# Performance work log

Measured on AMD Instinct MI355X. Metric: run time of the kernel, lower is better.

## Reference

```python
import jax, jax.numpy as jnp
import numpy as np

CODEBOOK_SIZE = 65536
HIDDEN = 768
B, L = 2, 2048
COMMITMENT_COST = 0.25


def setup_inputs() -> dict:
    key = jax.random.key(0)
    k1, k2 = jax.random.split(key)
    embeddings = jax.random.normal(k1, (B, L, HIDDEN), dtype=jnp.float32)
    # torch init: uniform(-1/K, 1/K)
    bound = 1.0 / CODEBOOK_SIZE
    codebook = jax.random.uniform(k2, (CODEBOOK_SIZE, HIDDEN), dtype=jnp.float32,
                                  minval=-bound, maxval=bound)
    return {"embeddings": embeddings, "codebook": codebook}


def reference(embeddings, codebook):
    Bv, Lv, D = embeddings.shape
    z = embeddings.reshape(-1, D)  # (N, D)
    # pairwise squared distances: z^2 + e^2 - 2 z e^T  -> (N, K)
    z_sq = jnp.sum(z * z, axis=-1, keepdims=True)          # (N, 1)
    e_sq = jnp.sum(codebook * codebook, axis=-1)[None, :]  # (1, K)
    distances = z_sq + e_sq - 2.0 * (z @ codebook.T)       # (N, K)
    codes = jnp.argmin(distances, axis=-1)                 # (N,)
    quantized = codebook[codes]                            # (N, D) gather
    # VQ loss: codebook loss + commitment loss (stop-grads as in torch .detach())
    codebook_loss = jnp.mean((quantized - jax.lax.stop_gradient(z)) ** 2)
    commitment_loss = jnp.mean((z - jax.lax.stop_gradient(quantized)) ** 2)
    vq_loss = codebook_loss + COMMITMENT_COST * commitment_loss
    # straight-through estimator
    quantized_ste = z + jax.lax.stop_gradient(quantized - z)
    return (codes.reshape(Bv, Lv),
            quantized_ste.reshape(Bv, Lv, D),
            vq_loss)
```

## Files before the change

kernel.cpp:

```cpp
#include <hip/hip_runtime.h>
#include <cfloat>
#include <cstdint>

#define NROWS  4096
#define DIM    768
#define KCODES 65536

#define TM 128
#define TC 128
#define BK1 128
#define SA 40
#define CAP 1024
#define DELTA 3.0e-4f

#define WS_ZSQ    0
#define WS_RUNMIN 16384
#define WS_CNT    32768
#define WS_CODESI 49152
#define WS_LOSS   65536
#define WS_LIST   131072
#define WS_AH     (WS_LIST + (size_t)NROWS*CAP*4)
#define WS_BH     (WS_AH + (size_t)NROWS*DIM*2)
#define WS_NEED   (WS_BH + (size_t)KCODES*DIM*2)

typedef _Float16 half_t;
typedef _Float16 half8 __attribute__((ext_vector_type(8)));
typedef float    f32x4 __attribute__((ext_vector_type(4)));

__device__ __forceinline__ void gld16(half_t* lds, const half_t* g) {
  __builtin_amdgcn_global_load_lds(
      (const __attribute__((address_space(1))) unsigned int*)g,
      (__attribute__((address_space(3))) unsigned int*)lds, 16, 0, 0);
}

__global__ void k0_zsq(const float* __restrict__ z, float* __restrict__ zsq,
                       unsigned int* __restrict__ runmin, int* __restrict__ cnt,
                       unsigned long long* __restrict__ keys, double* __restrict__ loss) {
  const int wave = threadIdx.x >> 6, lane = threadIdx.x & 63;
  const int row = blockIdx.x * 4 + wave;
  const float* zr = z + (size_t)row * DIM;
  float s = 0.f;
  #pragma unroll
  for (int i = 0; i < DIM / 64; ++i) { float v = zr[lane + i * 64]; s = fmaf(v, v, s); }
  #pragma unroll
  for (int off = 32; off; off >>= 1) s += __shfl_xor(s, off, 64);
  if (lane == 0) zsq[row] = s;
  const int gid = blockIdx.x * 256 + threadIdx.x;
  if (gid < NROWS) {
    runmin[gid] = 0x7f7fffffu;
    cnt[gid] = 0;
    keys[gid] = ~0ull;
  }
  if (gid == 0) *loss = 0.0;
}

__global__ void k_conv(const float* __restrict__ src, half_t* __restrict__ h,
                       int n8, float prescale) {
  const int i = blockIdx.x * 256 + threadIdx.x;
  if (i >= n8) return;
  float4 v0 = ((const float4*)src)[2 * i];
  float4 v1 = ((const float4*)src)[2 * i + 1];
  float a[8] = {v0.x, v0.y, v0.z, v0.w, v1.x, v1.y, v1.z, v1.w};
  half8 hi;
  #pragma unroll
  for (int j = 0; j < 8; ++j) hi[j] = (half_t)(a[j] * prescale);
  ((half8*)h)[i] = hi;
}

__global__ __launch_bounds__(256, 2) void k1_s1(
    const half_t* __restrict__ Ahg, const half_t* __restrict__ Bhg,
    const float* __restrict__ zsq, unsigned int* __restrict__ runmin,
    int* __restrict__ cnt, int* __restrict__ list) {
  __shared__ __align__(16) half_t sA[TM * BK1];
  __shared__ __align__(16) half_t sB[TC * BK1];
  __shared__ float lzs[TM];
  __shared__ float redD[TM][2];
  __shared__ float lbound[TM];

  const int tid = threadIdx.x;
  const int row0  = blockIdx.x * TM;
  const int code0 = blockIdx.y * TC;
  const int wave = tid >> 6, lane = tid & 63;
  const int wm = wave & 1, wn = wave >> 1;
  const int q = lane >> 4, l16 = lane & 15;

  if (tid < TM) lzs[tid] = zsq[row0 + tid];

  f32x4 acc[16];
  #pragma unroll
  for (int i = 0; i < 16; ++i) acc[i] = (f32x4){0.f, 0.f, 0.f, 0.f};

  for (int kd = 0; kd < DIM; kd += BK1) {
    __syncthreads();
    #pragma unroll
    for (int i = 0; i < 8; ++i) {
      const int sid  = i * 256 + tid;
      const int lrow = sid >> 4;
      const int kp   = sid & 15;
      const int klog = kp ^ (lrow & 7);
      const int loff = lrow * BK1 + kp * 8;
      gld16(&sA[loff], Ahg + (size_t)(row0 + lrow) * DIM + kd + klog * 8);
      gld16(&sB[loff], Bhg + (size_t)(code0 + lrow) * DIM + kd + klog * 8);
    }
    __syncthreads();

    #pragma unroll
    for (int s = 0; s < 4; ++s) {
      const int klq = s * 4 + q;
      half8 fa[4], fb[4];
      #pragma unroll
      for (int t = 0; t < 4; ++t) {
        const int ar = wm * 64 + t * 16 + l16;
        fa[t] = *(const half8*)&sA[ar * BK1 + (klq ^ (ar & 7)) * 8];
        const int br = wn * 64 + t * 16 + l16;
        fb[t] = *(const half8*)&sB[br * BK1 + (klq ^ (br & 7)) * 8];
      }
      #pragma unroll
      for (int tm = 0; tm < 4; ++tm)
        #pragma unroll
        for (int tn = 0; tn < 4; ++tn)
          acc[tm * 4 + tn] = __builtin_amdgcn_mfma_f32_16x16x32_f16(fa[tm], fb[tn], acc[tm * 4 + tn], 0, 0, 0);
    }
  }

  const float c2 = -4.8828125e-4f;
  #pragma unroll
  for (int tm = 0; tm < 4; ++tm)
    #pragma unroll
    for (int reg = 0; reg < 4; ++reg) {
      const float zs = lzs[wm * 64 + tm * 16 + q * 4 + reg];
      #pragma unroll
      for (int tn = 0; tn < 4; ++tn)
        acc[tm * 4 + tn][reg] = fmaf(c2, acc[tm * 4 + tn][reg], zs);
    }

  #pragma unroll
  for (int tm = 0; tm < 4; ++tm)
    #pragma unroll
    for (int reg = 0; reg < 4; ++reg) {
      float m = acc[tm * 4 + 0][reg];
      #pragma unroll
      for (int tn = 1; tn < 4; ++tn) m = fminf(m, acc[tm * 4 + tn][reg]);
      #pragma unroll
      for (int off = 8; off; off >>= 1) m = fminf(m, __shfl_xor(m, off, 64));
      if (l16 == 0) redD[wm * 64 + tm * 16 + q * 4 + reg][wn] = m;
    }
  __syncthreads();
  if (tid < TM) {
    const float lm = fminf(redD[tid][0], redD[tid][1]);
    const unsigned rg = runmin[row0 + tid];
    atomicMin(&runmin[row0 + tid], __float_as_uint(lm));
    lbound[tid] = fminf(lm, __uint_as_float(rg)) + DELTA;
  }
  __syncthreads();

  #pragma unroll
  for (int tm = 0; tm < 4; ++tm)
    #pragma unroll
    for (int reg = 0; reg < 4; ++reg) {
      const int row_b = wm * 64 + tm * 16 + q * 4 + reg;
      const float b = lbound[row_b];
      #pragma unroll
      for (int tn = 0; tn < 4; ++tn) {
        const float d = acc[tm * 4 + tn][reg];
        if (d <= b) {
          const int grow = row0 + row_b;
          const int pos = atomicAdd(&cnt[grow], 1);
          if (pos < CAP) list[(size_t)grow * CAP + pos] = code0 + wn * 64 + tn * 16 + l16;
        }
      }
    }
}

__global__ void k_refine(const float* __restrict__ z, const float* __restrict__ cb,
                         const float* __restrict__ zsq, const int* __restrict__ cnt,
                         const int* __restrict__ list, float* __restrict__ out_codes,
                         int* __restrict__ codes_i) {
  const int r = blockIdx.x;
  const int wave = threadIdx.x >> 6, lane = threadIdx.x & 63;
  __shared__ unsigned long long wbest[4];
  int n = cnt[r]; if (n > CAP) n = CAP;
  const bool empty = (n == 0); if (empty) n = 1;
  unsigned long long best = ~0ull;
  const float* zr = z + (size_t)r * DIM;
  for (int ci = wave; ci < n; ci += 4) {
    const int idx = empty ? 0 : list[(size_t)r * CAP + ci];
    const float* cr = cb + (size_t)idx * DIM;
    double s = 0.0;
    #pragma unroll
    for (int j = 0; j < 12; ++j) {
      const int k = lane + j * 64;
      s += (double)zr[k] * (double)cr[k];
    }
    #pragma unroll
    for (int off = 32; off; off >>= 1) s += __shfl_xor(s, off, 64);
    const float d = (float)((double)zsq[r] - 2.0 * s);
    const unsigned long long key =
        ((unsigned long long)__float_as_uint(d) << 32) | (unsigned)idx;
    if (key < best) best = key;
  }
  if (lane == 0) wbest[wave] = best;
  __syncthreads();
  if (threadIdx.x == 0) {
    unsigned long long b = wbest[0];
    #pragma unroll
    for (int w = 1; w < 4; ++w) if (wbest[w] < b) b = wbest[w];
    const int idx = (int)(unsigned)(b & 0xffffffffull);
    codes_i[r] = idx;
    out_codes[r] = (float)idx;
  }
}

__global__ __launch_bounds__(256, 2) void k1_mfma(
    const float* __restrict__ z, const float* __restrict__ cb,
    const float* __restrict__ zsq, unsigned long long* __restrict__ keys) {
  __shared__ half_t Ah[TM * SA], Al[TM * SA], Bh[TC * SA], Bl[TC * SA];
  __shared__ float lzs[TM];
  __shared__ float redD[TM][2];
  __shared__ int   redI[TM][2];

  const int tid  = threadIdx.x;
  const int row0  = blockIdx.x * TM;
  const int code0 = blockIdx.y * TC;
  const int wave = tid >> 6, lane = tid & 63;
  const int wm = wave & 1, wn = wave >> 1;
  const int q = lane >> 4, l16 = lane & 15;

  if (tid < TM) lzs[tid] = zsq[row0 + tid];

  const int srow = tid >> 2;
  const int sko  = (tid & 3) * 8;

  f32x4 acc0[16], acc1[16];
  #pragma unroll
  for (int i = 0; i < 16; ++i) {
    acc0[i] = (f32x4){0.f, 0.f, 0.f, 0.f};
    acc1[i] = (f32x4){0.f, 0.f, 0.f, 0.f};
  }

  const float* zp = z  + (size_t)row0  * DIM;
  const float* bp = cb + (size_t)code0 * DIM;

  for (int kd = 0; kd < DIM; kd += 32) {
    __syncthreads();
    #pragma unroll
    for (int s = 0; s < 2; ++s) {
      const int r = srow + s * 64;
      const float* srca = zp + (size_t)r * DIM + kd + sko;
      float4 v0 = *(const float4*)srca;
      float4 v1 = *(const float4*)(srca + 4);
      float a[8] = {v0.x, v0.y, v0.z, v0.w, v1.x, v1.y, v1.z, v1.w};
      half8 hi, lo;
      #pragma unroll
      for (int j = 0; j < 8; ++j) {
        half_t h = (half_t)a[j];
        hi[j] = h;
        lo[j] = (half_t)((a[j] - (float)h) * 4096.f);
      }
      *(half8*)&Ah[r * SA + sko] = hi;
      *(half8*)&Al[r * SA + sko] = lo;
      const float* srcb = bp + (size_t)r * DIM + kd + sko;
      v0 = *(const float4*)srcb; v1 = *(const float4*)(srcb + 4);
      float b[8] = {v0.x, v0.y, v0.z, v0.w, v1.x, v1.y, v1.z, v1.w};
      #pragma unroll
      for (int j = 0; j < 8; ++j) {
        float bs = b[j] * 4096.f;
        half_t h = (half_t)bs;
        hi[j] = h;
        lo[j] = (half_t)((bs - (float)h) * 4096.f);
      }
      *(half8*)&Bh[r * SA + sko] = hi;
      *(half8*)&Bl[r * SA + sko] = lo;
    }
    __syncthreads();

    half8 fa_h[4], fa_l[4], fb_h[4], fb_l[4];
    #pragma unroll
    for (int t = 0; t < 4; ++t) {
      const int ar = (wm * 64 + t * 16 + l16) * SA + q * 8;
      fa_h[t] = *(const half8*)&Ah[ar];
      fa_l[t] = *(const half8*)&Al[ar];
      const int br = (wn * 64 + t * 16 + l16) * SA + q * 8;
      fb_h[t] = *(const half8*)&Bh[br];
      fb_l[t] = *(const half8*)&Bl[br];
    }
    #pragma unroll
    for (int tm = 0; tm < 4; ++tm)
      #pragma unroll
      for (int tn = 0; tn < 4; ++tn) {
        const int i = tm * 4 + tn;
        acc0[i] = __builtin_amdgcn_mfma_f32_16x16x32_f16(fa_h[tm], fb_h[tn], acc0[i], 0, 0, 0);
        acc1[i] = __builtin_amdgcn_mfma_f32_16x16x32_f16(fa_l[tm], fb_h[tn], acc1[i], 0, 0, 0);
        acc1[i] = __builtin_amdgcn_mfma_f32_16x16x32_f16(fa_h[tm], fb_l[tn], acc1[i], 0, 0, 0);
      }
  }

  const float c1 = 2.44140625e-4f;
  const float c2 = -4.8828125e-4f;
  #pragma unroll
  for (int tm = 0; tm < 4; ++tm) {
    #pragma unroll
    for (int reg = 0; reg < 4; ++reg) {
      const int row_b = wm * 64 + tm * 16 + q * 4 + reg;
      const float zs = lzs[row_b];
      float bd = FLT_MAX; int bi = 0x7fffffff;
      #pragma unroll
      for (int tn = 0; tn < 4; ++tn) {
        const int i = tm * 4 + tn;
        float v = fmaf(c1, acc1[i][reg], acc0[i][reg]);
        float d = fmaf(c2, v, zs);
        const int ci = code0 + wn * 64 + tn * 16 + l16;
        if (d < bd || (d == bd && ci < bi)) { bd = d; bi = ci; }
      }
      #pragma unroll
      for (int off = 8; off; off >>= 1) {
        float od = __shfl_xor(bd, off, 64);
        int   oi = __shfl_xor(bi, off, 64);
        if (od < bd || (od == bd && oi < bi)) { bd = od; bi = oi; }
      }
      if (l16 == 0) { redD[row_b][wn] = bd; redI[row_b][wn] = bi; }
    }
  }
  __syncthreads();
  if (tid < TM) {
    float d0 = redD[tid][0]; int i0 = redI[tid][0];
    float d1 = redD[tid][1]; int i1 = redI[tid][1];
    if (d1 < d0 || (d1 == d0 && i1 < i0)) { d0 = d1; i0 = i1; }
    unsigned long long key = ((unsigned long long)__float_as_uint(d0) << 32) | (unsigned int)i0;
    atomicMin(&keys[row0 + tid], key);
  }
}

__global__ void k2_codes(const unsigned long long* __restrict__ keys,
                         float* __restrict__ out_codes, int* __restrict__ codes_i) {
  const int r = blockIdx.x * 256 + threadIdx.x;
  const int idx = (int)(unsigned int)(keys[r] & 0xffffffffull);
  out_codes[r] = (float)idx;
  codes_i[r] = idx;
}

__global__ void k3_quant_loss(const float* __restrict__ z, const float* __restrict__ cb,
                              const int* __restrict__ codes, float* __restrict__ outq,
                              double* __restrict__ loss) {
  const int gid = blockIdx.x * blockDim.x + threadIdx.x;
  const int e0 = gid * 4;
  const int row = e0 / DIM;
  const int col = e0 - row * DIM;
  const int c = codes[row];
  const float4 zv = *(const float4*)(z + e0);
  const float4 qv = *(const float4*)(cb + (size_t)c * DIM + col);
  float d0 = qv.x - zv.x, d1 = qv.y - zv.y, d2 = qv.z - zv.z, d3 = qv.w - zv.w;
  float4 ov = { zv.x + d0, zv.y + d1, zv.z + d2, zv.w + d3 };
  *(float4*)(outq + e0) = ov;
  double s = (double)(d0 * d0) + (double)(d1 * d1) + (double)(d2 * d2) + (double)(d3 * d3);
  #pragma unroll
  for (int off = 32; off; off >>= 1) s += __shfl_xor(s, off, 64);
  __shared__ double wsum[4];
  const int wave = threadIdx.x >> 6, lane = threadIdx.x & 63;
  if (lane == 0) wsum[wave] = s;
  __syncthreads();
  if (threadIdx.x == 0) atomicAdd(loss, wsum[0] + wsum[1] + wsum[2] + wsum[3]);
}

__global__ void k4_final(const double* __restrict__ loss, float* __restrict__ out) {
  float m = (float)(*loss / ((double)NROWS * (double)DIM));
  out[0] = m + 0.25f * m;
}

extern "C" void kernel_launch(void* const* d_in, const int* in_sizes, int n_in,
                              void* d_out, int out_size, void* d_ws, size_t ws_size,
                              hipStream_t stream) {
  const float* z  = (const float*)d_in[0];
  const float* cb = (const float*)d_in[1];
  float* out = (float*)d_out;
  char* ws = (char*)d_ws;
  float*  zsq = (float*)(ws + WS_ZSQ);
  unsigned int* runmin = (unsigned int*)(ws + WS_RUNMIN);
  int* cnt     = (int*)(ws + WS_CNT);
  int* codes_i = (int*)(ws + WS_CODESI);
  double* loss = (double*)(ws + WS_LOSS);
  int* list    = (int*)(ws + WS_LIST);
  unsigned long long* keys = (unsigned long long*)(ws + WS_LIST);

  k0_zsq<<<NROWS / 4, 256, 0, stream>>>(z, zsq, runmin, cnt, keys, loss);

  dim3 g1(NROWS / TM, KCODES / TC);
  if (ws_size >= WS_NEED) {
    half_t* Ahg = (half_t*)(ws + WS_AH);
    half_t* Bhg = (half_t*)(ws + WS_BH);
    k_conv<<<(NROWS * DIM / 8 + 255) / 256, 256, 0, stream>>>(z, Ahg, NROWS * DIM / 8, 1.0f);
    k_conv<<<(KCODES * DIM / 8 + 255) / 256, 256, 0, stream>>>(cb, Bhg, KCODES * DIM / 8, 4096.0f);
    k1_s1<<<g1, 256, 0, stream>>>(Ahg, Bhg, zsq, runmin, cnt, list);
    k_refine<<<NROWS, 256, 0, stream>>>(z, cb, zsq, cnt, list, out, codes_i);
  } else {
    k1_mfma<<<g1, 256, 0, stream>>>(z, cb, zsq, keys);
    k2_codes<<<NROWS / 256, 256, 0, stream>>>(keys, out, codes_i);
  }

  k3_quant_loss<<<(NROWS * DIM / 4) / 256, 256, 0, stream>>>(z, cb, codes_i, out + NROWS, loss);

  k4_final<<<1, 1, 0, stream>>>(loss, out + NROWS + (size_t)NROWS * DIM);
}
```

Baseline: 1.115 ms.

## Fuse zsq with z conversion, shrink GEMM K-tile, fuse quantize/loss into refine

The z-squared-norm pass now also converts z to fp16, which removes a separate conversion launch. The refine kernel now writes the straight-through quantized output and accumulates the loss itself, which removes the separate quantize/loss kernel. The screening GEMM uses a 64-wide K tile with a new swizzled load mapping and launch bounds raised to 4 blocks per CU, halving LDS per block so more blocks can be resident. The candidate list cap doubles, and refine stages the z row in LDS and uses float4 loads. Risks are register spilling at the higher occupancy target and more loop iterations and syncs per K step.

```diff
diff --git a/kernel.cpp b/kernel.cpp
--- a/kernel.cpp
+++ b/kernel.cpp
@@ -8,9 +8,9 @@
 
 #define TM 128
 #define TC 128
-#define BK1 128
+#define BK 64
 #define SA 40
-#define CAP 1024
+#define CAP 2048
 #define DELTA 3.0e-4f
 
 #define WS_ZSQ    0
@@ -24,6 +24,7 @@
 #define WS_NEED   (WS_BH + (size_t)KCODES*DIM*2)
 
 typedef _Float16 half_t;
+typedef _Float16 half4 __attribute__((ext_vector_type(4)));
 typedef _Float16 half8 __attribute__((ext_vector_type(8)));
 typedef float    f32x4 __attribute__((ext_vector_type(4)));
 
@@ -33,29 +34,31 @@
       (__attribute__((address_space(3))) unsigned int*)lds, 16, 0, 0);
 }
 
-__global__ void k0_zsq(const float* __restrict__ z, float* __restrict__ zsq,
-                       unsigned int* __restrict__ runmin, int* __restrict__ cnt,
-                       unsigned long long* __restrict__ keys, double* __restrict__ loss) {
+__global__ void k_convA(const float* __restrict__ z, half_t* __restrict__ h,
+                        float* __restrict__ zsq, unsigned int* __restrict__ runmin,
+                        int* __restrict__ cnt, double* __restrict__ loss) {
   const int wave = threadIdx.x >> 6, lane = threadIdx.x & 63;
   const int row = blockIdx.x * 4 + wave;
-  const float* zr = z + (size_t)row * DIM;
+  const float4* zr = (const float4*)(z + (size_t)row * DIM);
+  half_t* hr = h + (size_t)row * DIM;
   float s = 0.f;
   #pragma unroll
-  for (int i = 0; i < DIM / 64; ++i) { float v = zr[lane + i * 64]; s = fmaf(v, v, s); }
+  for (int p = 0; p < 3; ++p) {
+    float4 v = zr[lane + p * 64];
+    s = fmaf(v.x, v.x, s); s = fmaf(v.y, v.y, s);
+    s = fmaf(v.z, v.z, s); s = fmaf(v.w, v.w, s);
+    half4 hv = { (half_t)v.x, (half_t)v.y, (half_t)v.z, (half_t)v.w };
+    *(half4*)(hr + (lane + p * 64) * 4) = hv;
+  }
   #pragma unroll
   for (int off = 32; off; off >>= 1) s += __shfl_xor(s, off, 64);
   if (lane == 0) zsq[row] = s;
   const int gid = blockIdx.x * 256 + threadIdx.x;
-  if (gid < NROWS) {
-    runmin[gid] = 0x7f7fffffu;
-    cnt[gid] = 0;
-    keys[gid] = ~0ull;
-  }
+  if (gid < NROWS) { runmin[gid] = 0x7f7fffffu; cnt[gid] = 0; }
   if (gid == 0) *loss = 0.0;
 }
 
-__global__ void k_conv(const float* __restrict__ src, half_t* __restrict__ h,
-                       int n8, float prescale) {
+__global__ void k_convB(const float* __restrict__ src, half_t* __restrict__ h, int n8) {
   const int i = blockIdx.x * 256 + threadIdx.x;
   if (i >= n8) return;
   float4 v0 = ((const float4*)src)[2 * i];
@@ -63,16 +66,16 @@
   float a[8] = {v0.x, v0.y, v0.z, v0.w, v1.x, v1.y, v1.z, v1.w};
   half8 hi;
   #pragma unroll
-  for (int j = 0; j < 8; ++j) hi[j] = (half_t)(a[j] * prescale);
+  for (int j = 0; j < 8; ++j) hi[j] = (half_t)(a[j] * 4096.f);
   ((half8*)h)[i] = hi;
 }
 
-__global__ __launch_bounds__(256, 2) void k1_s1(
+__global__ __launch_bounds__(256, 4) void k1_s1(
     const half_t* __restrict__ Ahg, const half_t* __restrict__ Bhg,
     const float* __restrict__ zsq, unsigned int* __restrict__ runmin,
     int* __restrict__ cnt, int* __restrict__ list) {
-  __shared__ __align__(16) half_t sA[TM * BK1];
-  __shared__ __align__(16) half_t sB[TC * BK1];
+  __shared__ __align__(16) half_t sA[TM * BK];
+  __shared__ __align__(16) half_t sB[TC * BK];
   __shared__ float lzs[TM];
   __shared__ float redD[TM][2];
   __shared__ float lbound[TM];
@@ -86,34 +89,35 @@
 
   if (tid < TM) lzs[tid] = zsq[row0 + tid];
 
+  const int sr = lane >> 3;
+  const int ss = lane & 7;
+  const int gswz = ss ^ sr;
+
   f32x4 acc[16];
   #pragma unroll
   for (int i = 0; i < 16; ++i) acc[i] = (f32x4){0.f, 0.f, 0.f, 0.f};
 
-  for (int kd = 0; kd < DIM; kd += BK1) {
+  for (int kd = 0; kd < DIM; kd += BK) {
     __syncthreads();
     #pragma unroll
-    for (int i = 0; i < 8; ++i) {
-      const int sid  = i * 256 + tid;
-      const int lrow = sid >> 4;
-      const int kp   = sid & 15;
-      const int klog = kp ^ (lrow & 7);
-      const int loff = lrow * BK1 + kp * 8;
-      gld16(&sA[loff], Ahg + (size_t)(row0 + lrow) * DIM + kd + klog * 8);
-      gld16(&sB[loff], Bhg + (size_t)(code0 + lrow) * DIM + kd + klog * 8);
+    for (int i = 0; i < 4; ++i) {
+      const int r = wave * 32 + i * 8 + sr;
+      const int loff = r * BK + ss * 8;
+      gld16(&sA[loff], Ahg + (size_t)(row0  + r) * DIM + kd + gswz * 8);
+      gld16(&sB[loff], Bhg + (size_t)(code0 + r) * DIM + kd + gswz * 8);
     }
     __syncthreads();
 
     #pragma unroll
-    for (int s = 0; s < 4; ++s) {
+    for (int s = 0; s < 2; ++s) {
       const int klq = s * 4 + q;
       half8 fa[4], fb[4];
       #pragma unroll
       for (int t = 0; t < 4; ++t) {
         const int ar = wm * 64 + t * 16 + l16;
-        fa[t] = *(const half8*)&sA[ar * BK1 + (klq ^ (ar & 7)) * 8];
+        fa[t] = *(const half8*)&sA[ar * BK + ((klq ^ (ar & 7)) * 8)];
         const int br = wn * 64 + t * 16 + l16;
-        fb[t] = *(const half8*)&sB[br * BK1 + (klq ^ (br & 7)) * 8];
+        fb[t] = *(const half8*)&sB[br * BK + ((klq ^ (br & 7)) * 8)];
       }
       #pragma unroll
       for (int tm = 0; tm < 4; ++tm)
@@ -175,40 +179,88 @@
 __global__ void k_refine(const float* __restrict__ z, const float* __restrict__ cb,
                          const float* __restrict__ zsq, const int* __restrict__ cnt,
                          const int* __restrict__ list, float* __restrict__ out_codes,
-                         int* __restrict__ codes_i) {
+                         float* __restrict__ outq, double* __restrict__ loss) {
   const int r = blockIdx.x;
-  const int wave = threadIdx.x >> 6, lane = threadIdx.x & 63;
+  const int tid = threadIdx.x, wave = tid >> 6, lane = tid & 63;
   __shared__ unsigned long long wbest[4];
+  __shared__ double wsum[4];
+  __shared__ int sidx;
+  __shared__ __align__(16) float zsh[DIM];
+
+  if (tid < DIM / 4) ((float4*)zsh)[tid] = ((const float4*)(z + (size_t)r * DIM))[tid];
+  __syncthreads();
+
   int n = cnt[r]; if (n > CAP) n = CAP;
   const bool empty = (n == 0); if (empty) n = 1;
+  const double zsd = (double)zsq[r];
   unsigned long long best = ~0ull;
-  const float* zr = z + (size_t)r * DIM;
   for (int ci = wave; ci < n; ci += 4) {
     const int idx = empty ? 0 : list[(size_t)r * CAP + ci];
-    const float* cr = cb + (size_t)idx * DIM;
+    const float4* cr = (const float4*)(cb + (size_t)idx * DIM);
     double s = 0.0;
     #pragma unroll
-    for (int j = 0; j < 12; ++j) {
-      const int k = lane + j * 64;
-      s += (double)zr[k] * (double)cr[k];
+    for (int p = 0; p < 3; ++p) {
+      const float4 cv = cr[lane + p * 64];
+      const float4 zv = ((const float4*)zsh)[lane + p * 64];
+      s += (double)zv.x * cv.x + (double)zv.y * cv.y +
+           (double)zv.z * cv.z + (double)zv.w * cv.w;
     }
     #pragma unroll
     for (int off = 32; off; off >>= 1) s += __shfl_xor(s, off, 64);
-    const float d = (float)((double)zsq[r] - 2.0 * s);
+    const float d = (float)(zsd - 2.0 * s);
     const unsigned long long key =
         ((unsigned long long)__float_as_uint(d) << 32) | (unsigned)idx;
     if (key < best) best = key;
   }
   if (lane == 0) wbest[wave] = best;
   __syncthreads();
-  if (threadIdx.x == 0) {
+  if (tid == 0) {
     unsigned long long b = wbest[0];
     #pragma unroll
     for (int w = 1; w < 4; ++w) if (wbest[w] < b) b = wbest[w];
     const int idx = (int)(unsigned)(b & 0xffffffffull);
-    codes_i[r] = idx;
+    sidx = idx;
     out_codes[r] = (float)idx;
   }
+  __syncthreads();
+
+  const int c = sidx;
+  double ls = 0.0;
+  #pragma unroll
+  for (int j = 0; j < 3; ++j) {
+    const int e = tid + j * 256;
+    const float qx = cb[(size_t)c * DIM + e];
+    const float zx = zsh[e];
+    const float dd = qx - zx;
+    outq[(size_t)r * DIM + e] = zx + dd;
+    ls += (double)dd * (double)dd;
+  }
+  #pragma unroll
+  for (int off = 32; off; off >>= 1) ls += __shfl_xor(ls, off, 64);
+  if (lane == 0) wsum[wave] = ls;
+  __syncthreads();
+  if (tid == 0) atomicAdd(loss, wsum[0] + wsum[1] + wsum[2] + wsum[3]);
+}
+
+__global__ void k4_final(const double* __restrict__ loss, float* __restrict__ out) {
+  float m = (float)(*loss / ((double)NROWS * (double)DIM));
+  out[0] = m + 0.25f * m;
+}
+
+__global__ void k0_zsq(const float* __restrict__ z, float* __restrict__ zsq,
+                       unsigned long long* __restrict__ keys, double* __restrict__ loss) {
+  const int wave = threadIdx.x >> 6, lane = threadIdx.x & 63;
+  const int row = blockIdx.x * 4 + wave;
+  const float* zr = z + (size_t)row * DIM;
+  float s = 0.f;
+  #pragma unroll
+  for (int i = 0; i < DIM / 64; ++i) { float v = zr[lane + i * 64]; s = fmaf(v, v, s); }
+  #pragma unroll
+  for (int off = 32; off; off >>= 1) s += __shfl_xor(s, off, 64);
+  if (lane == 0) zsq[row] = s;
+  const int gid = blockIdx.x * 256 + threadIdx.x;
+  if (gid < NROWS) keys[gid] = ~0ull;
+  if (gid == 0) *loss = 0.0;
 }
 
 __global__ __launch_bounds__(256, 2) void k1_mfma(
@@ -362,11 +414,6 @@
   if (threadIdx.x == 0) atomicAdd(loss, wsum[0] + wsum[1] + wsum[2] + wsum[3]);
 }
 
-__global__ void k4_final(const double* __restrict__ loss, float* __restrict__ out) {
-  float m = (float)(*loss / ((double)NROWS * (double)DIM));
-  out[0] = m + 0.25f * m;
-}
-
 extern "C" void kernel_launch(void* const* d_in, const int* in_sizes, int n_in,
                               void* d_out, int out_size, void* d_ws, size_t ws_size,
                               hipStream_t stream) {
@@ -382,22 +429,21 @@
   int* list    = (int*)(ws + WS_LIST);
   unsigned long long* keys = (unsigned long long*)(ws + WS_LIST);
 
-  k0_zsq<<<NROWS / 4, 256, 0, stream>>>(z, zsq, runmin, cnt, keys, loss);
-
   dim3 g1(NROWS / TM, KCODES / TC);
+
   if (ws_size >= WS_NEED) {
     half_t* Ahg = (half_t*)(ws + WS_AH);
     half_t* Bhg = (half_t*)(ws + WS_BH);
-    k_conv<<<(NROWS * DIM / 8 + 255) / 256, 256, 0, stream>>>(z, Ahg, NROWS * DIM / 8, 1.0f);
-    k_conv<<<(KCODES * DIM / 8 + 255) / 256, 256, 0, stream>>>(cb, Bhg, KCODES * DIM / 8, 4096.0f);
+    k_convA<<<NROWS / 4, 256, 0, stream>>>(z, Ahg, zsq, runmin, cnt, loss);
+    k_convB<<<(KCODES * DIM / 8 + 255) / 256, 256, 0, stream>>>(cb, Bhg, KCODES * DIM / 8);
     k1_s1<<<g1, 256, 0, stream>>>(Ahg, Bhg, zsq, runmin, cnt, list);
-    k_refine<<<NROWS, 256, 0, stream>>>(z, cb, zsq, cnt, list, out, codes_i);
+    k_refine<<<NROWS, 256, 0, stream>>>(z, cb, zsq, cnt, list, out, out + NROWS, loss);
   } else {
+    k0_zsq<<<NROWS / 4, 256, 0, stream>>>(z, zsq, keys, loss);
     k1_mfma<<<g1, 256, 0, stream>>>(z, cb, zsq, keys);
     k2_codes<<<NROWS / 256, 256, 0, stream>>>(keys, out, codes_i);
-  }
-
-  k3_quant_loss<<<(NROWS * DIM / 4) / 256, 256, 0, stream>>>(z, cb, codes_i, out + NROWS, loss);
+    k3_quant_loss<<<(NROWS * DIM / 4) / 256, 256, 0, stream>>>(z, cb, codes_i, out + NROWS, loss);
+  }
 
   k4_final<<<1, 1, 0, stream>>>(loss, out + NROWS + (size_t)NROWS * DIM);
 }
```

New measurement: 928.1 us. 1.2x faster.
